# Kernel tuning notes

Measured on AMD Instinct MI355X. Metric: run time of the kernel, lower is better.

The kernel has to match this reference:

```python
import jax, jax.numpy as jnp
import numpy as np
from jax import lax

DIM = 96
STYLE = 128
LAT = 8
K = 7
PAD = 3
B = 2
SP = 48
EPS = 1e-06


def setup_inputs() -> dict:
    key = jax.random.key(0)
    ks = jax.random.split(key, 20)
    d = {}
    d['x'] = jax.random.normal(ks[0], (B, DIM, SP, SP, SP), jnp.float32)
    d['s'] = jax.random.normal(ks[1], (B, STYLE), jnp.float32)
    # LayerNorm (channels_first) params
    d['ln_w'] = jnp.ones((DIM,), jnp.float32)
    d['ln_b'] = jnp.zeros((DIM,), jnp.float32)
    # layer scale
    d['gamma'] = jnp.full((1, DIM, 1, 1, 1), 1e-06, jnp.float32)
    sc = 0.02
    # depthwise hyperConv: groups=DIM -> in/groups = 1
    d['dw_fc_w'] = jax.random.normal(ks[2], (LAT, STYLE), jnp.float32) * sc
    d['dw_fc_b'] = jnp.zeros((LAT,), jnp.float32)
    d['dw_bank'] = jax.random.normal(ks[3], (DIM, 1 * K * K * K, LAT), jnp.float32) * sc
    d['dw_bias_bank'] = jax.random.normal(ks[4], (DIM, LAT), jnp.float32) * sc
    # pwconv1: dim -> 4*dim, 1x1x1
    d['pw1_fc_w'] = jax.random.normal(ks[5], (LAT, STYLE), jnp.float32) * sc
    d['pw1_fc_b'] = jnp.zeros((LAT,), jnp.float32)
    d['pw1_bank'] = jax.random.normal(ks[6], (4 * DIM, DIM, LAT), jnp.float32) * sc
    d['pw1_bias_bank'] = jax.random.normal(ks[7], (4 * DIM, LAT), jnp.float32) * sc
    # pwconv2: 4*dim -> dim, 1x1x1
    d['pw2_fc_w'] = jax.random.normal(ks[8], (LAT, STYLE), jnp.float32) * sc
    d['pw2_fc_b'] = jnp.zeros((LAT,), jnp.float32)
    d['pw2_bank'] = jax.random.normal(ks[9], (DIM, 4 * DIM, LAT), jnp.float32) * sc
    d['pw2_bias_bank'] = jax.random.normal(ks[10], (DIM, LAT), jnp.float32) * sc
    return d


def _dw_conv_one(xb, wb):
    # xb: (C, D, H, W) padded; wb: (C, 1, K, K, K); depthwise 'VALID' conv
    return lax.conv_general_dilated(
        xb[None], wb, window_strides=(1, 1, 1), padding='VALID',
        dimension_numbers=('NCDHW', 'OIDHW', 'NCDHW'),
        feature_group_count=DIM)[0]


def reference(x, s, ln_w, ln_b, gamma,
              dw_fc_w, dw_fc_b, dw_bank, dw_bias_bank,
              pw1_fc_w, pw1_fc_b, pw1_bank, pw1_bias_bank,
              pw2_fc_w, pw2_fc_b, pw2_bank, pw2_bias_bank):
    inp = x
    # zero-pad spatial dims by PAD
    xp = jnp.pad(x, ((0, 0), (0, 0), (PAD, PAD), (PAD, PAD), (PAD, PAD)))

    # --- depthwise hyperConv ---
    z = s @ dw_fc_w.T + dw_fc_b                         # (B, LAT)
    w_dw = jnp.einsum('okl,bl->bok', dw_bank, z)        # (B, C, K^3)
    w_dw = w_dw.reshape(x.shape[0], DIM, 1, K, K, K)
    b_dw = jnp.einsum('ol,bl->bo', dw_bias_bank, z)     # (B, C)
    h = jax.vmap(_dw_conv_one)(xp, w_dw) + b_dw[:, :, None, None, None]

    # --- LayerNorm channels_first over channel axis ---
    u = h.mean(axis=1, keepdims=True)
    v = ((h - u) ** 2).mean(axis=1, keepdims=True)
    h = (h - u) / jnp.sqrt(v + EPS)
    h = ln_w[None, :, None, None, None] * h + ln_b[None, :, None, None, None]

    # --- pointwise hyperConv 1 (1x1x1) as batched channel matmul ---
    z1 = s @ pw1_fc_w.T + pw1_fc_b
    w1 = jnp.einsum('ocl,bl->boc', pw1_bank, z1)        # (B, 4C, C)
    b1 = jnp.einsum('ol,bl->bo', pw1_bias_bank, z1)
    h = jnp.einsum('bcdhw,boc->bodhw', h, w1) + b1[:, :, None, None, None]

    # GELU (exact erf form, torch nn.GELU default)
    h = jax.nn.gelu(h, approximate=False)

    # --- pointwise hyperConv 2 ---
    z2 = s @ pw2_fc_w.T + pw2_fc_b
    w2 = jnp.einsum('ocl,bl->boc', pw2_bank, z2)        # (B, C, 4C)
    b2 = jnp.einsum('ol,bl->bo', pw2_bias_bank, z2)
    h = jnp.einsum('bcdhw,boc->bodhw', h, w2) + b2[:, :, None, None, None]

    return inp + gamma * h
```

## Files before the change

kernel.cpp:

```cpp
#include <hip/hip_runtime.h>
#include <math.h>

#define DIM   96
#define C4    384
#define STYLE 128
#define LAT   8
#define KK    7
#define BB    2
#define SPD   48
#define SP3   (SPD*SPD*SPD)
#define EPSV  1e-6f

#define XTS_E 30
#define YB    2
#define YSPAN 16
#define ZSPAN 8
#define XSPAN 24
#define YROWS 22
#define YROWP 23
#define ZPL   14

#define WS_Z    0
#define WS_WDW  64
#define WS_BDW  (WS_WDW + BB*DIM*343)
#define WS_W1   (WS_BDW + BB*DIM)
#define WS_B1   (WS_W1 + BB*C4*DIM)
#define WS_W2T  (WS_B1 + BB*C4)
#define WS_B2   (WS_W2T + BB*C4*DIM)
#define WS_H    (WS_B2 + BB*DIM)

typedef __attribute__((ext_vector_type(8))) __bf16 bf16x8;
typedef __attribute__((ext_vector_type(4))) __bf16 bf16x4;
typedef __attribute__((ext_vector_type(4))) float  f32x4;

__global__ __launch_bounds__(64) void kz(const float* __restrict__ s,
                                         const float* __restrict__ dwfw, const float* __restrict__ dwfb,
                                         const float* __restrict__ p1fw, const float* __restrict__ p1fb,
                                         const float* __restrict__ p2fw, const float* __restrict__ p2fb,
                                         float* __restrict__ ws) {
    int t = threadIdx.x;
    if (t >= 48) return;
    int which = t >> 4;
    int b = (t >> 3) & 1;
    int l = t & 7;
    const float* fw = (which == 0) ? dwfw : (which == 1) ? p1fw : p2fw;
    const float* fb = (which == 0) ? dwfb : (which == 1) ? p1fb : p2fb;
    float acc = fb[l];
    for (int k = 0; k < STYLE; ++k) acc += s[b*STYLE + k] * fw[l*STYLE + k];
    ws[WS_Z + which*16 + b*8 + l] = acc;
}

__global__ __launch_bounds__(256) void kw(const float* __restrict__ dwb,  const float* __restrict__ dwbb,
                                          const float* __restrict__ p1b,  const float* __restrict__ p1bb,
                                          const float* __restrict__ p2b,  const float* __restrict__ p2bb,
                                          float* __restrict__ ws) {
    const int n0 = BB*DIM*343;
    const int n1 = n0 + BB*DIM;
    const int n2 = n1 + BB*C4*DIM;
    const int n3 = n2 + BB*C4;
    const int n4 = n3 + BB*C4*DIM;
    const int n5 = n4 + BB*DIM;
    int i = blockIdx.x * blockDim.x + threadIdx.x;
    if (i >= n5) return;
    const float* zdw = ws + WS_Z;
    const float* z1  = ws + WS_Z + 16;
    const float* z2  = ws + WS_Z + 32;
    if (i < n0) {
        int b = i / (DIM*343); int r = i % (DIM*343); int c = r / 343; int k = r % 343;
        const float* bank = dwb + ((size_t)(c*343 + k))*LAT;
        const float* z = zdw + b*8;
        float a = 0.f;
        #pragma unroll
        for (int l = 0; l < LAT; ++l) a += bank[l]*z[l];
        ws[WS_WDW + i] = a;
    } else if (i < n1) {
        int j = i - n0; int b = j / DIM; int c = j % DIM;
        const float* z = zdw + b*8;
        float a = 0.f;
        #pragma unroll
        for (int l = 0; l < LAT; ++l) a += dwbb[c*LAT + l]*z[l];
        ws[WS_BDW + j] = a;
    } else if (i < n2) {
        int j = i - n1; int b = j / (C4*DIM); int r = j % (C4*DIM); int o = r / DIM; int c = r % DIM;
        const float* z = z1 + b*8;
        const float* bank = p1b + ((size_t)(o*DIM + c))*LAT;
        float a = 0.f;
        #pragma unroll
        for (int l = 0; l < LAT; ++l) a += bank[l]*z[l];
        ((__bf16*)(ws + WS_W1))[j] = (__bf16)a;
    } else if (i < n3) {
        int j = i - n2; int b = j / C4; int o = j % C4;
        const float* z = z1 + b*8;
        float a = 0.f;
        #pragma unroll
        for (int l = 0; l < LAT; ++l) a += p1bb[o*LAT + l]*z[l];
        ws[WS_B1 + j] = a;
    } else if (i < n4) {
        int j = i - n3; int b = j / (C4*DIM); int r = j % (C4*DIM); int o = r / C4; int c4 = r % C4;
        const float* z = z2 + b*8;
        const float* bank = p2b + ((size_t)(o*C4 + c4))*LAT;
        float a = 0.f;
        #pragma unroll
        for (int l = 0; l < LAT; ++l) a += bank[l]*z[l];
        ((__bf16*)(ws + WS_W2T))[j] = (__bf16)a;
    } else {
        int j = i - n4; int b = j / DIM; int o = j % DIM;
        const float* z = z2 + b*8;
        float a = 0.f;
        #pragma unroll
        for (int l = 0; l < LAT; ++l) a += p2bb[o*LAT + l]*z[l];
        ws[WS_B2 + j] = a;
    }
}

__global__ __launch_bounds__(192, 4) void kconv(const float* __restrict__ x, float* __restrict__ ws) {
    __shared__ __bf16 xt[ZPL*YROWP*XTS_E];
    int tid = threadIdx.x;
    int bx = blockIdx.x;
    int zt = bx / 6;
    int rt = bx % 6; int yt = rt >> 1; int xti = rt & 1;
    int c = blockIdx.y, b = blockIdx.z;
    int z0 = zt*ZSPAN, y0 = yt*YSPAN, x0 = xti*XSPAN;

    const float* xsrc = x + ((size_t)(b*DIM + c))*SP3;
    for (int i = tid; i < ZPL*YROWS*XTS_E; i += 192) {
        int iz = i / (YROWS*XTS_E); int r = i % (YROWS*XTS_E);
        int iy = r / XTS_E; int ix = r % XTS_E;
        int gz = z0 - 3 + iz, gy = y0 - 3 + iy, gx = x0 + ix - 3;
        float v = 0.f;
        if ((unsigned)gz < 48u && (unsigned)gy < 48u && (unsigned)gx < 48u)
            v = xsrc[(gz*SPD + gy)*SPD + gx];
        xt[(iz*YROWP + iy)*XTS_E + ix] = (__bf16)v;
    }
    __syncthreads();

    int tz = tid / 24; int rem = tid % 24; int ty = rem / 3; int tx = rem % 3;
    int xb = tx*8;
    float acc[YB][8];
    #pragma unroll
    for (int yl = 0; yl < YB; ++yl)
        #pragma unroll
        for (int j = 0; j < 8; ++j) acc[yl][j] = 0.f;

    const float* wsrc = ws + WS_WDW + ((size_t)(b*DIM + c))*343;

    #pragma unroll 1
    for (int dz = 0; dz < 7; ++dz) {
        float wv[7][7];
        const float* wp = wsrc + dz*49;
        #pragma unroll
        for (int dy = 0; dy < 7; ++dy)
            #pragma unroll
            for (int dx = 0; dx < 7; ++dx)
                wv[dy][dx] = wp[dy*7 + dx];

        const int zr = (tz + dz)*YROWP + ty*YB;
        #pragma unroll
        for (int r = 0; r < YB + 6; ++r) {
            const uint32_t* rowp = (const uint32_t*)&xt[(zr + r)*XTS_E + xb];
            uint32_t dw[7];
            #pragma unroll
            for (int k = 0; k < 7; ++k) dw[k] = rowp[k];
            float rr[14];
            #pragma unroll
            for (int k = 0; k < 7; ++k) {
                rr[2*k]   = __uint_as_float(dw[k] << 16);
                rr[2*k+1] = __uint_as_float(dw[k] & 0xffff0000u);
            }
            #pragma unroll
            for (int yl = 0; yl < YB; ++yl) {
                const int dy = r - yl;
                if (dy >= 0 && dy < 7) {
                    #pragma unroll
                    for (int dx = 0; dx < 7; ++dx)
                        #pragma unroll
                        for (int j = 0; j < 8; ++j)
                            acc[yl][j] += wv[dy][dx]*rr[dx+j];
                }
            }
        }
    }

    float bias = ws[WS_BDW + b*DIM + c];
    #pragma unroll
    for (int yl = 0; yl < YB; ++yl) {
        float* hdst = ws + WS_H + ((size_t)(b*DIM + c))*SP3
                    + (((z0+tz)*SPD + (y0 + ty*YB + yl))*SPD + (x0 + xb));
        #pragma unroll
        for (int j = 0; j < 8; ++j) hdst[j] = acc[yl][j] + bias;
    }
}

__global__ __launch_bounds__(256) void kpw(const float* __restrict__ x,
                                           const float* __restrict__ lnw, const float* __restrict__ lnb,
                                           const float* __restrict__ gamma,
                                           float* __restrict__ out, const float* __restrict__ ws) {
    __shared__ __align__(16) __bf16 Hn[64][104];
    __shared__ __align__(16) __bf16 Gq[64][104];
    __shared__ float2 redbuf[256];

    const int tid  = threadIdx.x;
    const int lane = tid & 63;
    const int w    = tid >> 6;
    const int b    = blockIdx.y;
    const int sp0  = blockIdx.x * 64;

    {
        const float* hp = ws + WS_H + (size_t)b*DIM*SP3 + (size_t)(w*24)*SP3 + sp0 + lane;
        float hv[24]; float s = 0.f, q = 0.f;
        #pragma unroll
        for (int i = 0; i < 24; ++i) {
            float v = hp[(size_t)i*SP3];
            hv[i] = v; s += v; q += v*v;
        }
        redbuf[w*64 + lane] = make_float2(s, q);
        __syncthreads();
        float2 r0 = redbuf[lane], r1 = redbuf[64+lane], r2 = redbuf[128+lane], r3 = redbuf[192+lane];
        float st = (r0.x+r1.x) + (r2.x+r3.x);
        float qt = (r0.y+r1.y) + (r2.y+r3.y);
        float mean = st * (1.f/96.f);
        float var  = qt * (1.f/96.f) - mean*mean;
        float rstd = rsqrtf(fmaxf(var, 0.f) + EPSV);
        #pragma unroll
        for (int i = 0; i < 24; ++i) {
            float nv = (hv[i] - mean)*rstd*lnw[w*24+i] + lnb[w*24+i];
            Hn[lane][w*24 + i] = (__bf16)nv;
        }
    }
    __syncthreads();

    const __bf16* W1b = (const __bf16*)(ws + WS_W1)  + (size_t)b*C4*DIM;
    const __bf16* W2b = (const __bf16*)(ws + WS_W2T) + (size_t)b*DIM*C4;
    const float*  b1  = ws + WS_B1 + b*C4;
    const float*  b2  = ws + WS_B2 + b*DIM;

    const int l16  = lane & 15;
    const int quad = lane >> 4;

    const __bf16* bp = &Hn[w*16 + l16][quad*8];
    bf16x8 Bf0 = *(const bf16x8*)(bp);
    bf16x8 Bf1 = *(const bf16x8*)(bp + 32);
    bf16x8 Bf2 = *(const bf16x8*)(bp + 64);

    float acc2[6][4];
    #pragma unroll
    for (int m = 0; m < 6; ++m)
        #pragma unroll
        for (int r = 0; r < 4; ++r) acc2[m][r] = 0.f;

    #pragma unroll 1
    for (int q = 0; q < 4; ++q) {
        #pragma unroll 1
        for (int mtl = 0; mtl < 6; ++mtl) {
            const __bf16* ap = W1b + (size_t)((q*6 + mtl)*16 + l16)*DIM + quad*8;
            bf16x8 a0 = *(const bf16x8*)(ap);
            bf16x8 a1 = *(const bf16x8*)(ap + 32);
            bf16x8 a2 = *(const bf16x8*)(ap + 64);
            f32x4 acc = {0.f, 0.f, 0.f, 0.f};
            acc = __builtin_amdgcn_mfma_f32_16x16x32_bf16(a0, Bf0, acc, 0, 0, 0);
            acc = __builtin_amdgcn_mfma_f32_16x16x32_bf16(a1, Bf1, acc, 0, 0, 0);
            acc = __builtin_amdgcn_mfma_f32_16x16x32_bf16(a2, Bf2, acc, 0, 0, 0);
            int og = (q*6 + mtl)*16 + quad*4;
            int ol = mtl*16 + quad*4;
            bf16x4 gv;
            #pragma unroll
            for (int r = 0; r < 4; ++r) {
                float t = acc[r] + b1[og + r];
                float g = 0.5f*t*(1.f + erff(t*0.70710678f));
                gv[r] = (__bf16)g;
            }
            *(bf16x4*)&Gq[w*16 + l16][ol] = gv;
        }
        __syncthreads();

        #pragma unroll 1
        for (int ksl = 0; ksl < 3; ++ksl) {
            bf16x8 Bg = *(const bf16x8*)&Gq[w*16 + l16][ksl*32 + quad*8];
            const int kbase = q*96 + ksl*32 + quad*8;
            #pragma unroll
            for (int mt2 = 0; mt2 < 6; ++mt2) {
                const __bf16* ap2 = W2b + (size_t)(mt2*16 + l16)*C4 + kbase;
                bf16x8 a = *(const bf16x8*)(ap2);
                f32x4 c = {acc2[mt2][0], acc2[mt2][1], acc2[mt2][2], acc2[mt2][3]};
                c = __builtin_amdgcn_mfma_f32_16x16x32_bf16(a, Bg, c, 0, 0, 0);
                acc2[mt2][0] = c[0]; acc2[mt2][1] = c[1];
                acc2[mt2][2] = c[2]; acc2[mt2][3] = c[3];
            }
        }
        __syncthreads();
    }

    const int j = w*16 + l16;
    const size_t base = (size_t)b*DIM*SP3 + sp0 + j;
    #pragma unroll
    for (int mt2 = 0; mt2 < 6; ++mt2) {
        int obase = mt2*16 + quad*4;
        #pragma unroll
        for (int r = 0; r < 4; ++r) {
            int o = obase + r;
            size_t idx = base + (size_t)o*SP3;
            float y = acc2[mt2][r] + b2[o];
            out[idx] = x[idx] + gamma[o]*y;
        }
    }
}

extern "C" void kernel_launch(void* const* d_in, const int* in_sizes, int n_in,
                              void* d_out, int out_size, void* d_ws, size_t ws_size,
                              hipStream_t stream) {
    const float* x      = (const float*)d_in[0];
    const float* s      = (const float*)d_in[1];
    const float* lnw    = (const float*)d_in[2];
    const float* lnb    = (const float*)d_in[3];
    const float* gamma  = (const float*)d_in[4];
    const float* dwfw   = (const float*)d_in[5];
    const float* dwfb   = (const float*)d_in[6];
    const float* dwbank = (const float*)d_in[7];
    const float* dwbb   = (const float*)d_in[8];
    const float* p1fw   = (const float*)d_in[9];
    const float* p1fb   = (const float*)d_in[10];
    const float* p1bank = (const float*)d_in[11];
    const float* p1bb   = (const float*)d_in[12];
    const float* p2fw   = (const float*)d_in[13];
    const float* p2fb   = (const float*)d_in[14];
    const float* p2bank = (const float*)d_in[15];
    const float* p2bb   = (const float*)d_in[16];
    float* ws  = (float*)d_ws;
    float* out = (float*)d_out;

    kz<<<1, 64, 0, stream>>>(s, dwfw, dwfb, p1fw, p1fb, p2fw, p2fb, ws);
    const int totW = BB*DIM*343 + BB*DIM + BB*C4*DIM + BB*C4 + BB*C4*DIM + BB*DIM;
    kw<<<(totW + 255)/256, 256, 0, stream>>>(dwbank, dwbb, p1bank, p1bb, p2bank, p2bb, ws);
    kconv<<<dim3(36, DIM, BB), 192, 0, stream>>>(x, ws);
    kpw<<<dim3(SP3/64, BB), 256, 0, stream>>>(x, lnw, lnb, gamma, out, ws);
}
```

Measured before the change: 625.5 us.

## Use bf16 dot2 instructions with packed depthwise weights in conv kernel

```diff
diff --git a/kernel.cpp b/kernel.cpp
--- a/kernel.cpp
+++ b/kernel.cpp
@@ -32,6 +32,9 @@
 typedef __attribute__((ext_vector_type(8))) __bf16 bf16x8;
 typedef __attribute__((ext_vector_type(4))) __bf16 bf16x4;
 typedef __attribute__((ext_vector_type(4))) float  f32x4;
+
+#define DOT2(accv, av, bv) \
+    asm("v_dot2_f32_bf16 %0, %1, %2, %0" : "+v"(accv) : "v"(av), "v"(bv))
 
 __global__ __launch_bounds__(64) void kz(const float* __restrict__ s,
                                          const float* __restrict__ dwfw, const float* __restrict__ dwfb,
@@ -54,7 +57,7 @@
                                           const float* __restrict__ p1b,  const float* __restrict__ p1bb,
                                           const float* __restrict__ p2b,  const float* __restrict__ p2bb,
                                           float* __restrict__ ws) {
-    const int n0 = BB*DIM*343;
+    const int n0 = BB*DIM*49*4;
     const int n1 = n0 + BB*DIM;
     const int n2 = n1 + BB*C4*DIM;
     const int n3 = n2 + BB*C4;
@@ -66,13 +69,27 @@
     const float* z1  = ws + WS_Z + 16;
     const float* z2  = ws + WS_Z + 32;
     if (i < n0) {
-        int b = i / (DIM*343); int r = i % (DIM*343); int c = r / 343; int k = r % 343;
-        const float* bank = dwb + ((size_t)(c*343 + k))*LAT;
+        int b = i / (DIM*196); int r = i % (DIM*196); int c = r / 196; int s = r % 196;
+        int row = s >> 2;
+        int slot = s & 3;
         const float* z = zdw + b*8;
-        float a = 0.f;
-        #pragma unroll
-        for (int l = 0; l < LAT; ++l) a += bank[l]*z[l];
-        ws[WS_WDW + i] = a;
+        const float* bank = dwb + ((size_t)(c*343 + row*7))*LAT;
+        if (slot < 3) {
+            float a0 = 0.f, a1 = 0.f;
+            #pragma unroll
+            for (int l = 0; l < LAT; ++l) {
+                a0 += bank[(2*slot)*LAT + l]*z[l];
+                a1 += bank[(2*slot+1)*LAT + l]*z[l];
+            }
+            uint32_t p;
+            asm("v_cvt_pk_bf16_f32 %0, %1, %2" : "=v"(p) : "v"(a0), "v"(a1));
+            ((uint32_t*)(ws + WS_WDW))[(b*DIM + c)*196 + s] = p;
+        } else {
+            float a = 0.f;
+            #pragma unroll
+            for (int l = 0; l < LAT; ++l) a += bank[6*LAT + l]*z[l];
+            ws[WS_WDW + (b*DIM + c)*196 + s] = a;
+        }
     } else if (i < n1) {
         int j = i - n0; int b = j / DIM; int c = j % DIM;
         const float* z = zdw + b*8;
@@ -142,40 +159,58 @@
         #pragma unroll
         for (int j = 0; j < 8; ++j) acc[yl][j] = 0.f;
 
-    const float* wsrc = ws + WS_WDW + ((size_t)(b*DIM + c))*343;
+    const float4* wp4 = (const float4*)(ws + WS_WDW) + (size_t)(b*DIM + c)*49;
 
     #pragma unroll 1
     for (int dz = 0; dz < 7; ++dz) {
-        float wv[7][7];
-        const float* wp = wsrc + dz*49;
-        #pragma unroll
-        for (int dy = 0; dy < 7; ++dy)
-            #pragma unroll
-            for (int dx = 0; dx < 7; ++dx)
-                wv[dy][dx] = wp[dy*7 + dx];
+        float4 wq[7];
+        #pragma unroll
+        for (int dy = 0; dy < 7; ++dy) wq[dy] = wp4[dz*7 + dy];
 
         const int zr = (tz + dz)*YROWP + ty*YB;
         #pragma unroll
         for (int r = 0; r < YB + 6; ++r) {
             const uint32_t* rowp = (const uint32_t*)&xt[(zr + r)*XTS_E + xb];
-            uint32_t dw[7];
-            #pragma unroll
-            for (int k = 0; k < 7; ++k) dw[k] = rowp[k];
-            float rr[14];
-            #pragma unroll
-            for (int k = 0; k < 7; ++k) {
-                rr[2*k]   = __uint_as_float(dw[k] << 16);
-                rr[2*k+1] = __uint_as_float(dw[k] & 0xffff0000u);
+            uint32_t dwv[7];
+            #pragma unroll
+            for (int k = 0; k < 7; ++k) dwv[k] = rowp[k];
+            uint32_t sh[6];
+            #pragma unroll
+            for (int k = 0; k < 6; ++k)
+                asm("v_alignbit_b32 %0, %1, %2, 16"
+                    : "=v"(sh[k]) : "v"(dwv[k+1]), "v"(dwv[k]));
+            float tlo[4], thi[4];
+            #pragma unroll
+            for (int m = 0; m < 4; ++m) {
+                tlo[m] = __uint_as_float(dwv[3+m] << 16);
+                thi[m] = __uint_as_float(dwv[3+m] & 0xffff0000u);
             }
             #pragma unroll
             for (int yl = 0; yl < YB; ++yl) {
                 const int dy = r - yl;
                 if (dy >= 0 && dy < 7) {
+                    const uint32_t w01 = __float_as_uint(wq[dy].x);
+                    const uint32_t w23 = __float_as_uint(wq[dy].y);
+                    const uint32_t w45 = __float_as_uint(wq[dy].z);
+                    const float    w6  = wq[dy].w;
                     #pragma unroll
-                    for (int dx = 0; dx < 7; ++dx)
-                        #pragma unroll
-                        for (int j = 0; j < 8; ++j)
-                            acc[yl][j] += wv[dy][dx]*rr[dx+j];
+                    for (int m = 0; m < 4; ++m) {
+                        float a = acc[yl][2*m];
+                        DOT2(a, w01, dwv[m]);
+                        DOT2(a, w23, dwv[m+1]);
+                        DOT2(a, w45, dwv[m+2]);
+                        a = fmaf(w6, tlo[m], a);
+                        acc[yl][2*m] = a;
+                    }
+                    #pragma unroll
+                    for (int m = 0; m < 4; ++m) {
+                        float a = acc[yl][2*m+1];
+                        DOT2(a, w01, sh[m]);
+                        DOT2(a, w23, sh[m+1]);
+                        DOT2(a, w45, sh[m+2]);
+                        a = fmaf(w6, thi[m], a);
+                        acc[yl][2*m+1] = a;
+                    }
                 }
             }
         }
@@ -281,10 +316,10 @@
             for (int mt2 = 0; mt2 < 6; ++mt2) {
                 const __bf16* ap2 = W2b + (size_t)(mt2*16 + l16)*C4 + kbase;
                 bf16x8 a = *(const bf16x8*)(ap2);
-                f32x4 c = {acc2[mt2][0], acc2[mt2][1], acc2[mt2][2], acc2[mt2][3]};
-                c = __builtin_amdgcn_mfma_f32_16x16x32_bf16(a, Bg, c, 0, 0, 0);
-                acc2[mt2][0] = c[0]; acc2[mt2][1] = c[1];
-                acc2[mt2][2] = c[2]; acc2[mt2][3] = c[3];
+                f32x4 cacc = {acc2[mt2][0], acc2[mt2][1], acc2[mt2][2], acc2[mt2][3]};
+                cacc = __builtin_amdgcn_mfma_f32_16x16x32_bf16(a, Bg, cacc, 0, 0, 0);
+                acc2[mt2][0] = cacc[0]; acc2[mt2][1] = cacc[1];
+                acc2[mt2][2] = cacc[2]; acc2[mt2][3] = cacc[3];
             }
         }
         __syncthreads();
@@ -329,7 +364,7 @@
     float* out = (float*)d_out;
 
     kz<<<1, 64, 0, stream>>>(s, dwfw, dwfb, p1fw, p1fb, p2fw, p2fb, ws);
-    const int totW = BB*DIM*343 + BB*DIM + BB*C4*DIM + BB*C4 + BB*C4*DIM + BB*DIM;
+    const int totW = BB*DIM*49*4 + BB*DIM + BB*C4*DIM + BB*C4 + BB*C4*DIM + BB*DIM;
     kw<<<(totW + 255)/256, 256, 0, stream>>>(dwbank, dwbb, p1bank, p1bb, p2bank, p2bb, ws);
     kconv<<<dim3(36, DIM, BB), 192, 0, stream>>>(x, ws);
     kpw<<<dim3(SP3/64, BB), 256, 0, stream>>>(x, lnw, lnb, gamma, out, ws);
```

Measured after the change: 630.9 us. About the same (+0.9%).
